# Performance work log

Measured on AMD Instinct MI355X. Metric: run time of the kernel, lower is better.

The kernel has to match this reference:

```python
import jax, jax.numpy as jnp
import numpy as np
from jax import lax

LB, UB = 0.0, 0.1
N_ITERS = 32  # fixed-point iterations for water-filling rebalance


def _conv(x, w, b):
    y = lax.conv_general_dilated(x, w, (1, 1), ((1, 1), (1, 1)),
                                 dimension_numbers=("NCHW", "OIHW", "NCHW"))
    return y + b[None, :, None, None]


def _maxpool2(x):
    return lax.reduce_window(x, -jnp.inf, lax.max, (1, 1, 2, 2), (1, 1, 2, 2), "VALID")


def _linear(x, w, b):
    return x @ w.T + b


def _gru(x_num, W_ih, W_hh, b_ih, b_hh):
    # x_num: [B, S, N]; torch GRU gate order r, z, n
    B = x_num.shape[0]
    H = W_hh.shape[1]
    xs = jnp.swapaxes(x_num, 0, 1)  # [S, B, N]

    def step(h, x_t):
        gi = x_t @ W_ih.T + b_ih            # [B, 3H]
        gh = h @ W_hh.T + b_hh              # [B, 3H]
        i_r, i_z, i_n = jnp.split(gi, 3, axis=-1)
        h_r, h_z, h_n = jnp.split(gh, 3, axis=-1)
        r = jax.nn.sigmoid(i_r + h_r)
        z = jax.nn.sigmoid(i_z + h_z)
        n = jnp.tanh(i_n + r * h_n)
        h_new = (1.0 - z) * n + z * h
        return h_new, None

    h0 = jnp.zeros((B, H), dtype=x_num.dtype)
    h_last, _ = lax.scan(step, h0, xs)
    return h_last


def _rebalance_one(w):
    # vectorized fixed-point version of the per-sample while-loop water-filling
    def body(carry, _):
        old, wc = carry
        leftover = jnp.sum(old - wc)
        mask = wc != UB
        s = jnp.sum(jnp.where(mask, wc, 0.0))
        gift = jnp.where(mask & (s > 0), leftover * wc / jnp.where(s > 0, s, 1.0), 0.0)
        new_old = wc + gift
        new_wc = jnp.clip(new_old, LB, UB)
        return (new_old, new_wc), None

    init = (w, jnp.clip(w, LB, UB))
    (_, wc), _ = lax.scan(body, init, None, length=N_ITERS)
    return wc


def setup_inputs() -> dict:
    key = jax.random.key(0)
    ks = jax.random.split(key, 16)
    B, S, N, H_IMG, W_IMG, HID = 16, 60, 50, 64, 60, 128
    fc_in = 64 * (H_IMG // 4) * (W_IMG // 4)  # 15360
    sc = 0.05
    return {
        "x_num": jax.random.normal(ks[0], (B, S, N), jnp.float32),
        "x_img": jax.random.uniform(ks[1], (B, N, H_IMG, W_IMG), jnp.float32),
        "conv1_w": jax.random.normal(ks[2], (32, 1, 3, 3), jnp.float32) * sc,
        "conv1_b": jnp.zeros((32,), jnp.float32),
        "conv2_w": jax.random.normal(ks[3], (64, 32, 3, 3), jnp.float32) * sc,
        "conv2_b": jnp.zeros((64,), jnp.float32),
        "fc1_w": jax.random.normal(ks[4], (64, fc_in), jnp.float32) * 0.01,
        "fc1_b": jnp.zeros((64,), jnp.float32),
        "fc_binary_w": jax.random.normal(ks[5], (1, 64), jnp.float32) * sc,
        "fc_binary_b": jnp.zeros((1,), jnp.float32),
        "fc2_w": jax.random.normal(ks[6], (128, 64), jnp.float32) * sc,
        "fc2_b": jnp.zeros((128,), jnp.float32),
        "W_ih": jax.random.normal(ks[7], (3 * HID, N), jnp.float32) * sc,
        "W_hh": jax.random.normal(ks[8], (3 * HID, HID), jnp.float32) * sc,
        "b_ih": jnp.zeros((3 * HID,), jnp.float32),
        "b_hh": jnp.zeros((3 * HID,), jnp.float32),
        "gru_fc_w": jax.random.normal(ks[9], (N, HID), jnp.float32) * sc,
        "gru_fc_b": jnp.zeros((N,), jnp.float32),
        "fusion_w": jax.random.normal(ks[10], (64, N + 128), jnp.float32) * sc,
        "fusion_b": jnp.zeros((64,), jnp.float32),
        "final_w": jax.random.normal(ks[11], (N, 64), jnp.float32) * sc,
        "final_b": jnp.zeros((N,), jnp.float32),
    }


def reference(x_num, x_img, conv1_w, conv1_b, conv2_w, conv2_b, fc1_w, fc1_b,
              fc_binary_w, fc_binary_b, fc2_w, fc2_b, W_ih, W_hh, b_ih, b_hh,
              gru_fc_w, gru_fc_b, fusion_w, fusion_b, final_w, final_b):
    B, S, N = x_num.shape
    # GRU branch: last hidden -> Linear -> [B, N]
    h_last = _gru(x_num, W_ih, W_hh, b_ih, b_hh)
    numerical_features = _linear(h_last, gru_fc_w, gru_fc_b)

    # CNN branch on per-stock chart images
    xi = x_img.reshape(B * N, 1, x_img.shape[2], x_img.shape[3])
    h = _maxpool2(jax.nn.relu(_conv(xi, conv1_w, conv1_b)))
    h = _maxpool2(jax.nn.relu(_conv(h, conv2_w, conv2_b)))
    h = h.reshape(B * N, -1)
    feats = jax.nn.relu(_linear(h, fc1_w, fc1_b))
    binary_pred = jax.nn.sigmoid(_linear(feats, fc_binary_w, fc_binary_b))
    cnn_features = _linear(feats, fc2_w, fc2_b).reshape(B, N, -1).mean(axis=1)

    fused = jax.nn.relu(_linear(jnp.concatenate([numerical_features, cnn_features], axis=1), fusion_w, fusion_b))
    w = jax.nn.softmax(_linear(fused, final_w, final_b), axis=1)
    portfolio_weights = jax.vmap(_rebalance_one)(w)
    return portfolio_weights, binary_pred.reshape(B, N)
```

## Files before the change

### kernel.cpp

```cpp
#include <hip/hip_runtime.h>
#include <hip/hip_bf16.h>

typedef unsigned short ushort_t;
typedef short short8_t __attribute__((ext_vector_type(8)));
typedef float f32x4 __attribute__((ext_vector_type(4)));
typedef float f32x16 __attribute__((ext_vector_type(16)));
typedef ushort_t us4_t __attribute__((ext_vector_type(4)));

#define NBATCH 16
#define SEQ    60
#define NSTK   50
#define HID    128
#define G3     384
#define NIMG   800
#define IH     64
#define IW     60
#define P1H    32
#define P1W    30
#define P2C    64
#define FCIN   15360

#define OFF_WHHF   0u
#define OFF_WPREP  24576u
#define OFF_WFC1   33792u
#define OFF_GI     525312u
#define OFF_HLAST  893952u
#define OFF_POOL2  896000u
#define OFF_FC2O   7040000u
#define OFF_PART   7142400u
#define WS_FLOATS  7961600u

#define E_WHH  49152
#define E_WPR  18432
#define E_FC1  983040
#define E_TOT  (E_WHH + E_WPR + E_FC1)

struct __align__(16) ConvS {
    ushort_t pool1t[32][4][32][8];
    union {
        float    imgp[64][60];
        ushort_t pool2s[64][120];
    } u;
};
struct __align__(16) GruS {
    float    gh[16 * 388];
    ushort_t hb[16 * 136];
};
#define SMEM_BYTES 80896

__device__ __forceinline__ float fast_sig(float x) {
    const float e = __expf(-x);
    return __builtin_amdgcn_rcpf(1.f + e);
}
__device__ __forceinline__ float fast_tanh(float x) {
    const float xc = fmaxf(fminf(x, 15.f), -15.f);
    const float e = __expf(2.f * xc);
    return (e - 1.f) * __builtin_amdgcn_rcpf(e + 1.f);
}

__global__ __launch_bounds__(384) void k_pre(const float* __restrict__ xnum,
                                             const float* __restrict__ wih,
                                             const float* __restrict__ bih,
                                             const float* __restrict__ whh,
                                             const float* __restrict__ c2w,
                                             const float* __restrict__ fc1w,
                                             float* __restrict__ GI,
                                             ushort_t* __restrict__ whhf,
                                             ushort_t* __restrict__ wprep,
                                             ushort_t* __restrict__ wfc1)
{
    const int bid = blockIdx.x;
    if (bid < 960) {
        const int s = bid >> 4, b = bid & 15;
        const int j = threadIdx.x;
        const float* xr = xnum + (size_t)(b * SEQ + s) * NSTK;
        const float* wr = wih + (size_t)j * NSTK;
        float a = bih[j];
        #pragma unroll 10
        for (int k = 0; k < NSTK; ++k) a = fmaf(xr[k], wr[k], a);
        GI[((size_t)s * 16 + b) * G3 + j] = a;
        return;
    }
    const int idx = (bid - 960) * 384 + threadIdx.x;
    if (idx < E_WHH) {
        const int e = idx;
        const int i = e & 7, l = (e >> 3) & 63, ksj = e >> 9;
        const int ks = ksj & 3, jt = ksj >> 2;
        const int j = jt * 16 + (l & 15);
        const int k = ks * 32 + ((l >> 4) << 3) + i;
        __hip_bfloat16 hv = __float2bfloat16(whh[j * HID + k]);
        whhf[e] = *(ushort_t*)&hv;
    } else if (idx < E_WHH + E_WPR) {
        const int e = idx - E_WHH;
        const int i = e & 7, l = (e >> 3) & 63, rest = e >> 9;
        const int ks = rest & 1, mt = rest >> 1;
        const int tap = mt % 9, mm = mt / 9;
        const int oc = mm * 32 + (l & 31);
        const int ic = ks * 16 + ((l >> 5) << 3) + i;
        __hip_bfloat16 hv = __float2bfloat16(c2w[((size_t)oc * 32 + ic) * 9 + tap]);
        wprep[e] = *(ushort_t*)&hv;
    } else if (idx < E_TOT) {
        const int e = idx - (E_WHH + E_WPR);
        const int i = e & 7, l = (e >> 3) & 63, rest = e >> 9;
        const int n = rest & 3, T = rest >> 2;
        const int oc = n * 16 + (l & 15);
        const int k = T * 32 + ((l >> 4) << 3) + i;
        __hip_bfloat16 hv = __float2bfloat16(fc1w[(size_t)oc * FCIN + k]);
        wfc1[e] = *(ushort_t*)&hv;
    }
}

__global__ __launch_bounds__(512, 2) void k_mega(const float* __restrict__ x_img,
                                                 const float* __restrict__ c1w,
                                                 const float* __restrict__ c1b,
                                                 const float* __restrict__ c2b,
                                                 const ushort_t* __restrict__ wprep,
                                                 const float* __restrict__ GI,
                                                 const ushort_t* __restrict__ whhf,
                                                 const float* __restrict__ bhh,
                                                 ushort_t* __restrict__ pool2,
                                                 float* __restrict__ hlast)
{
    extern __shared__ char smraw[];
    const int tid = threadIdx.x;
    const int bid = blockIdx.x;

    if (bid == 0) {
        GruS* g = (GruS*)smraw;
        const int w = tid >> 6, l = tid & 63;
        const int arow = l & 15, kq = l >> 4;
        short8_t wfr[3][4];
        #pragma unroll
        for (int jj = 0; jj < 3; ++jj)
            #pragma unroll
            for (int ks = 0; ks < 4; ++ks)
                wfr[jj][ks] = *(const short8_t*)&whhf[((((w * 3 + jj) * 4 + ks) * 64 + l) * 8)];

        const int b = tid >> 5, hh0 = (tid & 31) * 4;
        const f32x4 bhr = *(const f32x4*)&bhh[hh0];
        const f32x4 bhz = *(const f32x4*)&bhh[128 + hh0];
        const f32x4 bhn = *(const f32x4*)&bhh[256 + hh0];
        float h0 = 0.f, h1 = 0.f, h2 = 0.f, h3 = 0.f;
        for (int i = tid; i < 1088; i += 512) ((unsigned int*)g->hb)[i] = 0u;
        const float* gi0 = GI + b * G3 + hh0;
        f32x4 cr = *(const f32x4*)(gi0);
        f32x4 cz = *(const f32x4*)(gi0 + 128);
        f32x4 cn = *(const f32x4*)(gi0 + 256);
        __syncthreads();

        for (int s = 0; s < SEQ; ++s) {
            const int sn = (s + 1 < SEQ) ? s + 1 : s;
            const float* gnx = GI + ((size_t)sn * 16 + b) * G3 + hh0;
            const f32x4 nr = *(const f32x4*)(gnx);
            const f32x4 nz = *(const f32x4*)(gnx + 128);
            const f32x4 nn = *(const f32x4*)(gnx + 256);

            #pragma unroll
            for (int jj = 0; jj < 3; ++jj) {
                f32x4 a = {0.f, 0.f, 0.f, 0.f};
                #pragma unroll
                for (int ks = 0; ks < 4; ++ks) {
                    short8_t af = *(const short8_t*)&g->hb[arow * 136 + ks * 32 + kq * 8];
                    a = __builtin_amdgcn_mfma_f32_16x16x32_bf16(af, wfr[jj][ks], a, 0, 0, 0);
                }
                const int jt = w * 3 + jj;
                #pragma unroll
                for (int r = 0; r < 4; ++r)
                    g->gh[(kq * 4 + r) * 388 + jt * 16 + arow] = a[r];
            }
            __syncthreads();

            const f32x4 gr = *(const f32x4*)&g->gh[b * 388 + hh0];
            const f32x4 gz = *(const f32x4*)&g->gh[b * 388 + 128 + hh0];
            const f32x4 gn = *(const f32x4*)&g->gh[b * 388 + 256 + hh0];
            float hv0, hv1, hv2, hv3;
            {
                const float r0 = fast_sig(cr[0] + gr[0] + bhr[0]);
                const float z0 = fast_sig(cz[0] + gz[0] + bhz[0]);
                const float n0 = fast_tanh(cn[0] + r0 * (gn[0] + bhn[0]));
                hv0 = (1.f - z0) * n0 + z0 * h0;
                const float r1 = fast_sig(cr[1] + gr[1] + bhr[1]);
                const float z1 = fast_sig(cz[1] + gz[1] + bhz[1]);
                const float n1 = fast_tanh(cn[1] + r1 * (gn[1] + bhn[1]));
                hv1 = (1.f - z1) * n1 + z1 * h1;
                const float r2 = fast_sig(cr[2] + gr[2] + bhr[2]);
                const float z2 = fast_sig(cz[2] + gz[2] + bhz[2]);
                const float n2 = fast_tanh(cn[2] + r2 * (gn[2] + bhn[2]));
                hv2 = (1.f - z2) * n2 + z2 * h2;
                const float r3 = fast_sig(cr[3] + gr[3] + bhr[3]);
                const float z3 = fast_sig(cz[3] + gz[3] + bhz[3]);
                const float n3 = fast_tanh(cn[3] + r3 * (gn[3] + bhn[3]));
                hv3 = (1.f - z3) * n3 + z3 * h3;
            }
            h0 = hv0; h1 = hv1; h2 = hv2; h3 = hv3;
            us4_t hp;
            { __hip_bfloat16 t0 = __float2bfloat16(h0); hp[0] = *(ushort_t*)&t0; }
            { __hip_bfloat16 t1 = __float2bfloat16(h1); hp[1] = *(ushort_t*)&t1; }
            { __hip_bfloat16 t2 = __float2bfloat16(h2); hp[2] = *(ushort_t*)&t2; }
            { __hip_bfloat16 t3 = __float2bfloat16(h3); hp[3] = *(ushort_t*)&t3; }
            *(us4_t*)&g->hb[b * 136 + hh0] = hp;
            cr = nr; cz = nz; cn = nn;
            __syncthreads();
        }
        f32x4 ho = {h0, h1, h2, h3};
        *(f32x4*)&hlast[b * HID + hh0] = ho;
        return;
    }

    ConvS* c = (ConvS*)smraw;
    const int img = bid - 1;
    const float* xim = x_img + (size_t)img * (IH * IW);

    if (tid < 256) {
        const int y = tid >> 3, cg = (tid >> 1) & 3, xs = (tid & 1) * 31;
        short8_t z = {0, 0, 0, 0, 0, 0, 0, 0};
        *(short8_t*)&c->pool1t[y][cg][xs][0] = z;
    }
    {
        const f32x4* src = (const f32x4*)xim;
        f32x4* dst = (f32x4*)c->u.imgp;
        for (int i = tid; i < 960; i += 512) dst[i] = src[i];
    }
    __syncthreads();

    #pragma unroll
    for (int rep = 0; rep < 2; ++rep) {
        const int p = tid + rep * 512;
        if (p < 960) {
            const int py = p / 30, px = p - py * 30;
            float patch[4][4];
            #pragma unroll
            for (int yy = 0; yy < 4; ++yy) {
                const int iy = 2 * py - 1 + yy;
                #pragma unroll
                for (int xx = 0; xx < 4; ++xx) {
                    const int ix = 2 * px - 1 + xx;
                    patch[yy][xx] = (iy >= 0 && iy < IH && ix >= 0 && ix < IW)
                                        ? c->u.imgp[iy][ix] : 0.f;
                }
            }
            #pragma unroll
            for (int cg = 0; cg < 4; ++cg) {
                short8_t outv;
                #pragma unroll
                for (int ch8 = 0; ch8 < 8; ++ch8) {
                    const int ch = cg * 8 + ch8;
                    float wr[9];
                    #pragma unroll
                    for (int q = 0; q < 9; ++q) wr[q] = c1w[ch * 9 + q];
                    const float bia = c1b[ch];
                    float best = 0.f;
                    #pragma unroll
                    for (int dy = 0; dy < 2; ++dy)
                        #pragma unroll
                        for (int dx = 0; dx < 2; ++dx) {
                            float sv = 0.f;
                            #pragma unroll
                            for (int ky = 0; ky < 3; ++ky)
                                #pragma unroll
                                for (int kx = 0; kx < 3; ++kx)
                                    sv = fmaf(patch[dy + ky][dx + kx], wr[ky * 3 + kx], sv);
                            best = fmaxf(best, sv + bia);
                        }
                    __hip_bfloat16 hv = __float2bfloat16(best);
                    outv[ch8] = *(short*)&hv;
                }
                *(short8_t*)&c->pool1t[py][cg][px + 1][0] = outv;
            }
        }
    }
    __syncthreads();

    {
        const int w  = tid >> 6, l = tid & 63;
        const int m  = w & 1;
        const int hi = l >> 5;
        const int col = l & 31;

        short8_t af[9][2];
        #pragma unroll
        for (int tap = 0; tap < 9; ++tap)
            #pragma unroll
            for (int ks = 0; ks < 2; ++ks)
                af[tap][ks] = *(const short8_t*)&wprep[(((m * 9 + tap) * 2 + ks) * 64 + l) * 8];
        float bia[16];
        #pragma unroll
        for (int r = 0; r < 16; ++r)
            bia[r] = c2b[m * 32 + (r & 3) + 8 * (r >> 2) + 4 * hi];

        const bool wr = ((col & 1) == 0) && (col < 30);
        const int px = col >> 1;
        const short8_t bfz = {0, 0, 0, 0, 0, 0, 0, 0};

        #pragma unroll
        for (int ph = 0; ph < 2; ++ph) {
            #pragma unroll
            for (int yy = 0; yy < 2; ++yy) {
                const int yp = ph * 8 + (w >> 1) + yy * 4;
                f32x16 a0, a1;
                #pragma unroll
                for (int r = 0; r < 16; ++r) { a0[r] = 0.f; a1[r] = 0.f; }
                #pragma unroll
                for (int ro = 0; ro < 4; ++ro) {
                    const int y = 2 * yp - 1 + ro;
                    short8_t bf[3][2];
                    if (y >= 0 && y < 32) {
                        #pragma unroll
                        for (int kx = 0; kx < 3; ++kx)
                            #pragma unroll
                            for (int ks = 0; ks < 2; ++ks)
                                bf[kx][ks] = *(const short8_t*)&c->pool1t[y][ks * 2 + hi][kx + col][0];
                    } else {
                        #pragma unroll
                        for (int kx = 0; kx < 3; ++kx)
                            #pragma unroll
                            for (int ks = 0; ks < 2; ++ks) bf[kx][ks] = bfz;
                    }
                    if (ro < 3) {
                        #pragma unroll
                        for (int kx = 0; kx < 3; ++kx)
                            #pragma unroll
                            for (int ks = 0; ks < 2; ++ks)
                                a0 = __builtin_amdgcn_mfma_f32_32x32x16_bf16(af[ro * 3 + kx][ks], bf[kx][ks], a0, 0, 0, 0);
                    }
                    if (ro >= 1) {
                        #pragma unroll
                        for (int kx = 0; kx < 3; ++kx)
                            #pragma unroll
                            for (int ks = 0; ks < 2; ++ks)
                                a1 = __builtin_amdgcn_mfma_f32_32x32x16_bf16(af[(ro - 1) * 3 + kx][ks], bf[kx][ks], a1, 0, 0, 0);
                    }
                }
                #pragma unroll
                for (int r = 0; r < 16; ++r) {
                    float v = fmaxf(a0[r], a1[r]);
                    v = fmaxf(v, __shfl_xor(v, 1, 64));
                    v = fmaxf(v + bia[r], 0.f);
                    if (wr) {
                        const int oc = m * 32 + (r & 3) + 8 * (r >> 2) + 4 * hi;
                        __hip_bfloat16 hv = __float2bfloat16(v);
                        c->u.pool2s[oc][(yp & 7) * 15 + px] = *(ushort_t*)&hv;
                    }
                }
            }
            __syncthreads();
            {
                int4* dst = (int4*)(pool2 + (size_t)img * FCIN);
                const int4* src = (const int4*)c->u.pool2s;
                #pragma unroll
                for (int jj = 0; jj < 2; ++jj) {
                    const int i = tid + jj * 512;
                    if (i < 960) {
                        const int oc = i / 15, cc = i - oc * 15;
                        dst[oc * 30 + ph * 15 + cc] = src[i];
                    }
                }
            }
            __syncthreads();
        }
    }
}

__global__ __launch_bounds__(256) void k_fc1(const ushort_t* __restrict__ pool2,
                                             const ushort_t* __restrict__ wfc1,
                                             float* __restrict__ part)
{
    const int mt = blockIdx.x >> 4;
    const int ks = blockIdx.x & 15;
    const int n = threadIdx.x >> 6, l = threadIdx.x & 63;
    const int arow = l & 15, kq = l >> 4;
    const int img16 = mt * 16;
    const ushort_t* Ab = pool2 + (size_t)(img16 + arow) * FCIN + ks * 960 + kq * 8;
    const ushort_t* Bb = wfc1 + ((size_t)(ks * 30 * 4 + n) * 64 + l) * 8;
    f32x4 acc0 = {0.f, 0.f, 0.f, 0.f}, acc1 = {0.f, 0.f, 0.f, 0.f};
    #pragma unroll 5
    for (int t = 0; t < 30; t += 2) {
        const short8_t aA = *(const short8_t*)(Ab + (size_t)t * 32);
        const short8_t bA = *(const short8_t*)(Bb + (size_t)t * 2048);
        const short8_t aB = *(const short8_t*)(Ab + (size_t)(t + 1) * 32);
        const short8_t bB = *(const short8_t*)(Bb + (size_t)(t + 1) * 2048);
        acc0 = __builtin_amdgcn_mfma_f32_16x16x32_bf16(aA, bA, acc0, 0, 0, 0);
        acc1 = __builtin_amdgcn_mfma_f32_16x16x32_bf16(aB, bB, acc1, 0, 0, 0);
    }
    float* dst = &part[((size_t)ks * NIMG + img16 + kq * 4) * 64 + n * 16 + arow];
    #pragma unroll
    for (int r = 0; r < 4; ++r)
        dst[(size_t)r * 64] = acc0[r] + acc1[r];
}

__device__ __forceinline__ float wave_sum(float v) {
    #pragma unroll
    for (int o = 32; o > 0; o >>= 1) v += __shfl_xor(v, o, 64);
    return v;
}
__device__ __forceinline__ float wave_max(float v) {
    #pragma unroll
    for (int o = 32; o > 0; o >>= 1) v = fmaxf(v, __shfl_xor(v, o, 64));
    return v;
}

__global__ __launch_bounds__(512) void k_post(const float* __restrict__ part,
                                              const float* __restrict__ fc1b,
                                              const float* __restrict__ fbw,
                                              const float* __restrict__ fbb,
                                              const float* __restrict__ fc2w,
                                              const float* __restrict__ fc2b,
                                              float* __restrict__ out,
                                              float* __restrict__ fc2o)
{
    const int t = threadIdx.x;
    const int im8 = t >> 6;
    const int tl = t & 63;
    const int img = blockIdx.x * 8 + im8;
    float s = fc1b[tl];
    #pragma unroll
    for (int ks = 0; ks < 16; ++ks) s += part[((size_t)ks * NIMG + img) * 64 + tl];
    const float f = fmaxf(s, 0.f);
    __shared__ float flc[8][64];
    flc[im8][tl] = f;
    const float bs = wave_sum(f * fbw[tl]);
    if (tl == 0) out[800 + img] = 1.f / (1.f + expf(-(bs + fbb[0])));
    __syncthreads();
    #pragma unroll
    for (int q = 0; q < 2; ++q) {
        const int j = tl + q * 64;
        float a2 = fc2b[j];
        #pragma unroll 8
        for (int k = 0; k < 64; ++k) a2 = fmaf(flc[im8][k], fc2w[j * 64 + k], a2);
        fc2o[(size_t)img * 128 + j] = a2;
    }
}

__global__ __launch_bounds__(64) void k_final(const float* __restrict__ hlast,
                                              const float* __restrict__ fc2o,
                                              const float* __restrict__ gw,
                                              const float* __restrict__ gb,
                                              const float* __restrict__ fw,
                                              const float* __restrict__ fb,
                                              const float* __restrict__ finw,
                                              const float* __restrict__ finb,
                                              float* __restrict__ out)
{
    const int b = blockIdx.x, t = threadIdx.x;
    __shared__ float cf[128], nf[64], fu[64];
    #pragma unroll
    for (int jj = 0; jj < 2; ++jj) {
        const int j = t + jj * 64;
        float s = 0.f;
        for (int n = 0; n < NSTK; ++n) s += fc2o[(size_t)(b * NSTK + n) * 128 + j];
        cf[j] = s * (1.0f / 50.0f);
    }
    float s = 0.f;
    if (t < NSTK) {
        s = gb[t];
        for (int k = 0; k < HID; ++k) s = fmaf(hlast[b * HID + k], gw[t * HID + k], s);
    }
    nf[t] = (t < NSTK) ? s : 0.f;
    __syncthreads();
    float f = fb[t];
    for (int k = 0; k < NSTK; ++k) f = fmaf(nf[k], fw[t * 178 + k], f);
    for (int k = 0; k < 128; ++k) f = fmaf(cf[k], fw[t * 178 + 50 + k], f);
    fu[t] = fmaxf(f, 0.f);
    __syncthreads();
    float L = -3.4e38f;
    if (t < NSTK) {
        L = finb[t];
        for (int k = 0; k < 64; ++k) L = fmaf(fu[k], finw[t * 64 + k], L);
    }
    const float m = wave_max(L);
    const float e = (t < NSTK) ? expf(L - m) : 0.f;
    const float se = wave_sum(e);
    const float wv = e / se;
    float old = wv;
    float wc = fminf(fmaxf(wv, 0.f), 0.1f);
    for (int it = 0; it < 32; ++it) {
        const float leftover = wave_sum(old - wc);
        const bool mask = (wc != 0.1f);
        const float ssum = wave_sum(mask ? wc : 0.f);
        const float gift = (mask && ssum > 0.f) ? leftover * wc / ssum : 0.f;
        old = wc + gift;
        wc = fminf(fmaxf(old, 0.f), 0.1f);
    }
    if (t < NSTK) out[b * NSTK + t] = wc;
}

extern "C" void kernel_launch(void* const* d_in, const int* in_sizes, int n_in,
                              void* d_out, int out_size, void* d_ws, size_t ws_size,
                              hipStream_t stream)
{
    const float* x_num = (const float*)d_in[0];
    const float* x_img = (const float*)d_in[1];
    const float* c1w  = (const float*)d_in[2];
    const float* c1b  = (const float*)d_in[3];
    const float* c2w  = (const float*)d_in[4];
    const float* c2b  = (const float*)d_in[5];
    const float* fc1w = (const float*)d_in[6];
    const float* fc1b = (const float*)d_in[7];
    const float* fbw  = (const float*)d_in[8];
    const float* fbb  = (const float*)d_in[9];
    const float* fc2w = (const float*)d_in[10];
    const float* fc2b = (const float*)d_in[11];
    const float* wih  = (const float*)d_in[12];
    const float* whh  = (const float*)d_in[13];
    const float* bih  = (const float*)d_in[14];
    const float* bhh  = (const float*)d_in[15];
    const float* gw   = (const float*)d_in[16];
    const float* gb   = (const float*)d_in[17];
    const float* fw   = (const float*)d_in[18];
    const float* fb   = (const float*)d_in[19];
    const float* finw = (const float*)d_in[20];
    const float* finb = (const float*)d_in[21];
    float* out = (float*)d_out;
    float* ws  = (float*)d_ws;
    if (ws_size < (size_t)WS_FLOATS * 4) return;

    ushort_t* whhf  = (ushort_t*)(ws + OFF_WHHF);
    ushort_t* wprep = (ushort_t*)(ws + OFF_WPREP);
    ushort_t* wfc1  = (ushort_t*)(ws + OFF_WFC1);
    float* GI       = ws + OFF_GI;
    float* hlast    = ws + OFF_HLAST;
    ushort_t* pool2 = (ushort_t*)(ws + OFF_POOL2);
    float* fc2o     = ws + OFF_FC2O;
    float* part     = ws + OFF_PART;

    (void)hipFuncSetAttribute(reinterpret_cast<const void*>(k_mega),
                              hipFuncAttributeMaxDynamicSharedMemorySize, SMEM_BYTES);

    k_pre   <<<960 + 2736, 384, 0, stream>>>(x_num, wih, bih, whh, c2w, fc1w,
                                             GI, whhf, wprep, wfc1);
    k_mega  <<<NIMG + 1, 512, SMEM_BYTES, stream>>>(x_img, c1w, c1b, c2b, wprep,
                                                    GI, whhf, bhh, pool2, hlast);
    k_fc1   <<<50 * 16, 256, 0, stream>>>(pool2, wfc1, part);
    k_post  <<<100, 512, 0, stream>>>(part, fc1b, fbw, fbb, fc2w, fc2b, out, fc2o);
    k_final <<<NBATCH, 64, 0, stream>>>(hlast, fc2o, gw, gb, fw, fb, finw, finb, out);
}
```

Before: 153.8 us.

## Split each image's conv pipeline across two blocks with halo rows

Each image is now handled by two blocks, each computing half of the pool2 rows. Each block loads only the input rows it needs plus halo rows and recomputes the overlapping pool1 halo row. Shared memory per block drops, so launch bounds ask for three blocks per CU instead of two. The aim is more parallelism and occupancy in the conv stage. The cost is redundant halo-row conv1 work, and the single GRU block now runs alongside twice as many conv blocks.

```diff
diff --git a/kernel.cpp b/kernel.cpp
--- a/kernel.cpp
+++ b/kernel.cpp
@@ -36,9 +36,9 @@
 #define E_TOT  (E_WHH + E_WPR + E_FC1)
 
 struct __align__(16) ConvS {
-    ushort_t pool1t[32][4][32][8];
+    ushort_t pool1t[18][4][32][8];
     union {
-        float    imgp[64][60];
+        float    imgp[35][60];
         ushort_t pool2s[64][120];
     } u;
 };
@@ -46,7 +46,7 @@
     float    gh[16 * 388];
     ushort_t hb[16 * 136];
 };
-#define SMEM_BYTES 80896
+#define SMEM_BYTES 52224
 
 __device__ __forceinline__ float fast_sig(float x) {
     const float e = __expf(-x);
@@ -110,7 +110,7 @@
     }
 }
 
-__global__ __launch_bounds__(512, 2) void k_mega(const float* __restrict__ x_img,
+__global__ __launch_bounds__(512, 3) void k_mega(const float* __restrict__ x_img,
                                                  const float* __restrict__ c1w,
                                                  const float* __restrict__ c1b,
                                                  const float* __restrict__ c2b,
@@ -208,65 +208,73 @@
     }
 
     ConvS* c = (ConvS*)smraw;
-    const int img = bid - 1;
+    const int img  = (bid - 1) >> 1;
+    const int half = (bid - 1) & 1;
     const float* xim = x_img + (size_t)img * (IH * IW);
-
-    if (tid < 256) {
-        const int y = tid >> 3, cg = (tid >> 1) & 3, xs = (tid & 1) * 31;
-        short8_t z = {0, 0, 0, 0, 0, 0, 0, 0};
-        *(short8_t*)&c->pool1t[y][cg][xs][0] = z;
-    }
+    const int rowbase = 29 * half;
+
     {
-        const f32x4* src = (const f32x4*)xim;
+        const short8_t z = {0, 0, 0, 0, 0, 0, 0, 0};
+        const int zrow = half ? 17 : 0;
+        if (tid < 128) {
+            const int cg = tid >> 5, xs = tid & 31;
+            *(short8_t*)&c->pool1t[zrow][cg][xs][0] = z;
+        } else if (tid < 272) {
+            const int q = tid - 128;
+            const int ly = q / 8, cg = (q >> 1) & 3, xs = (q & 1) * 31;
+            *(short8_t*)&c->pool1t[ly][cg][xs][0] = z;
+        }
+    }
+    {
+        const f32x4* src = (const f32x4*)(xim + rowbase * IW);
         f32x4* dst = (f32x4*)c->u.imgp;
-        for (int i = tid; i < 960; i += 512) dst[i] = src[i];
+        for (int i = tid; i < 525; i += 512) dst[i] = src[i];
     }
     __syncthreads();
 
-    #pragma unroll
-    for (int rep = 0; rep < 2; ++rep) {
-        const int p = tid + rep * 512;
-        if (p < 960) {
-            const int py = p / 30, px = p - py * 30;
-            float patch[4][4];
-            #pragma unroll
-            for (int yy = 0; yy < 4; ++yy) {
-                const int iy = 2 * py - 1 + yy;
+    if (tid < 510) {
+        const int gj = tid / 30, px = tid - gj * 30;
+        const int g = half * 15 + gj;
+        const int ly = gj + 1 - half;
+        float patch[4][4];
+        #pragma unroll
+        for (int yy = 0; yy < 4; ++yy) {
+            const int giy = 2 * g - 1 + yy;
+            const int liy = giy - rowbase;
+            #pragma unroll
+            for (int xx = 0; xx < 4; ++xx) {
+                const int ix = 2 * px - 1 + xx;
+                patch[yy][xx] = (giy >= 0 && giy < IH && ix >= 0 && ix < IW)
+                                    ? c->u.imgp[liy][ix] : 0.f;
+            }
+        }
+        #pragma unroll
+        for (int cg = 0; cg < 4; ++cg) {
+            short8_t outv;
+            #pragma unroll
+            for (int ch8 = 0; ch8 < 8; ++ch8) {
+                const int ch = cg * 8 + ch8;
+                float wr[9];
                 #pragma unroll
-                for (int xx = 0; xx < 4; ++xx) {
-                    const int ix = 2 * px - 1 + xx;
-                    patch[yy][xx] = (iy >= 0 && iy < IH && ix >= 0 && ix < IW)
-                                        ? c->u.imgp[iy][ix] : 0.f;
-                }
-            }
-            #pragma unroll
-            for (int cg = 0; cg < 4; ++cg) {
-                short8_t outv;
+                for (int q = 0; q < 9; ++q) wr[q] = c1w[ch * 9 + q];
+                const float bia = c1b[ch];
+                float best = 0.f;
                 #pragma unroll
-                for (int ch8 = 0; ch8 < 8; ++ch8) {
-                    const int ch = cg * 8 + ch8;
-                    float wr[9];
+                for (int dy = 0; dy < 2; ++dy)
                     #pragma unroll
-                    for (int q = 0; q < 9; ++q) wr[q] = c1w[ch * 9 + q];
-                    const float bia = c1b[ch];
-                    float best = 0.f;
-                    #pragma unroll
-                    for (int dy = 0; dy < 2; ++dy)
+                    for (int dx = 0; dx < 2; ++dx) {
+                        float sv = 0.f;
                         #pragma unroll
-                        for (int dx = 0; dx < 2; ++dx) {
-                            float sv = 0.f;
+                        for (int ky = 0; ky < 3; ++ky)
                             #pragma unroll
-                            for (int ky = 0; ky < 3; ++ky)
-                                #pragma unroll
-                                for (int kx = 0; kx < 3; ++kx)
-                                    sv = fmaf(patch[dy + ky][dx + kx], wr[ky * 3 + kx], sv);
-                            best = fmaxf(best, sv + bia);
-                        }
-                    __hip_bfloat16 hv = __float2bfloat16(best);
-                    outv[ch8] = *(short*)&hv;
-                }
-                *(short8_t*)&c->pool1t[py][cg][px + 1][0] = outv;
-            }
+                            for (int kx = 0; kx < 3; ++kx)
+                                sv = fmaf(patch[dy + ky][dx + kx], wr[ky * 3 + kx], sv);
+                        best = fmaxf(best, sv + bia);
+                    }
+                __hip_bfloat16 hv = __float2bfloat16(best);
+                outv[ch8] = *(short*)&hv;
+            }
+            *(short8_t*)&c->pool1t[ly][cg][px + 1][0] = outv;
         }
     }
     __syncthreads();
@@ -290,73 +298,61 @@
 
         const bool wr = ((col & 1) == 0) && (col < 30);
         const int px = col >> 1;
-        const short8_t bfz = {0, 0, 0, 0, 0, 0, 0, 0};
 
         #pragma unroll
-        for (int ph = 0; ph < 2; ++ph) {
-            #pragma unroll
-            for (int yy = 0; yy < 2; ++yy) {
-                const int yp = ph * 8 + (w >> 1) + yy * 4;
-                f32x16 a0, a1;
+        for (int yy = 0; yy < 2; ++yy) {
+            const int ypl = (w >> 1) + yy * 4;
+            f32x16 a0, a1;
+            #pragma unroll
+            for (int r = 0; r < 16; ++r) { a0[r] = 0.f; a1[r] = 0.f; }
+            #pragma unroll
+            for (int ro = 0; ro < 4; ++ro) {
+                const int ly = 2 * ypl + ro;
+                short8_t bf[3][2];
                 #pragma unroll
-                for (int r = 0; r < 16; ++r) { a0[r] = 0.f; a1[r] = 0.f; }
-                #pragma unroll
-                for (int ro = 0; ro < 4; ++ro) {
-                    const int y = 2 * yp - 1 + ro;
-                    short8_t bf[3][2];
-                    if (y >= 0 && y < 32) {
+                for (int kx = 0; kx < 3; ++kx)
+                    #pragma unroll
+                    for (int ks = 0; ks < 2; ++ks)
+                        bf[kx][ks] = *(const short8_t*)&c->pool1t[ly][ks * 2 + hi][kx + col][0];
+                if (ro < 3) {
+                    #pragma unroll
+                    for (int kx = 0; kx < 3; ++kx)
                         #pragma unroll
-                        for (int kx = 0; kx < 3; ++kx)
-                            #pragma unroll
-                            for (int ks = 0; ks < 2; ++ks)
-                                bf[kx][ks] = *(const short8_t*)&c->pool1t[y][ks * 2 + hi][kx + col][0];
-                    } else {
+                        for (int ks = 0; ks < 2; ++ks)
+                            a0 = __builtin_amdgcn_mfma_f32_32x32x16_bf16(af[ro * 3 + kx][ks], bf[kx][ks], a0, 0, 0, 0);
+                }
+                if (ro >= 1) {
+                    #pragma unroll
+                    for (int kx = 0; kx < 3; ++kx)
                         #pragma unroll
-                        for (int kx = 0; kx < 3; ++kx)
-                            #pragma unroll
-                            for (int ks = 0; ks < 2; ++ks) bf[kx][ks] = bfz;
-                    }
-                    if (ro < 3) {
-                        #pragma unroll
-                        for (int kx = 0; kx < 3; ++kx)
-                            #pragma unroll
-                            for (int ks = 0; ks < 2; ++ks)
-                                a0 = __builtin_amdgcn_mfma_f32_32x32x16_bf16(af[ro * 3 + kx][ks], bf[kx][ks], a0, 0, 0, 0);
-                    }
-                    if (ro >= 1) {
-                        #pragma unroll
-                        for (int kx = 0; kx < 3; ++kx)
-                            #pragma unroll
-                            for (int ks = 0; ks < 2; ++ks)
-                                a1 = __builtin_amdgcn_mfma_f32_32x32x16_bf16(af[(ro - 1) * 3 + kx][ks], bf[kx][ks], a1, 0, 0, 0);
-                    }
+                        for (int ks = 0; ks < 2; ++ks)
+                            a1 = __builtin_amdgcn_mfma_f32_32x32x16_bf16(af[(ro - 1) * 3 + kx][ks], bf[kx][ks], a1, 0, 0, 0);
                 }
-                #pragma unroll
-                for (int r = 0; r < 16; ++r) {
-                    float v = fmaxf(a0[r], a1[r]);
-                    v = fmaxf(v, __shfl_xor(v, 1, 64));
-                    v = fmaxf(v + bia[r], 0.f);
-                    if (wr) {
-                        const int oc = m * 32 + (r & 3) + 8 * (r >> 2) + 4 * hi;
-                        __hip_bfloat16 hv = __float2bfloat16(v);
-                        c->u.pool2s[oc][(yp & 7) * 15 + px] = *(ushort_t*)&hv;
-                    }
+            }
+            #pragma unroll
+            for (int r = 0; r < 16; ++r) {
+                float v = fmaxf(a0[r], a1[r]);
+                v = fmaxf(v, __shfl_xor(v, 1, 64));
+                v = fmaxf(v + bia[r], 0.f);
+                if (wr) {
+                    const int oc = m * 32 + (r & 3) + 8 * (r >> 2) + 4 * hi;
+                    __hip_bfloat16 hv = __float2bfloat16(v);
+                    c->u.pool2s[oc][ypl * 15 + px] = *(ushort_t*)&hv;
                 }
             }
-            __syncthreads();
-            {
-                int4* dst = (int4*)(pool2 + (size_t)img * FCIN);
-                const int4* src = (const int4*)c->u.pool2s;
-                #pragma unroll
-                for (int jj = 0; jj < 2; ++jj) {
-                    const int i = tid + jj * 512;
-                    if (i < 960) {
-                        const int oc = i / 15, cc = i - oc * 15;
-                        dst[oc * 30 + ph * 15 + cc] = src[i];
-                    }
+        }
+        __syncthreads();
+        {
+            int4* dst = (int4*)(pool2 + (size_t)img * FCIN);
+            const int4* src = (const int4*)c->u.pool2s;
+            #pragma unroll
+            for (int jj = 0; jj < 2; ++jj) {
+                const int i = tid + jj * 512;
+                if (i < 960) {
+                    const int oc = i / 15, cc = i - oc * 15;
+                    dst[oc * 30 + half * 15 + cc] = src[i];
                 }
             }
-            __syncthreads();
         }
     }
 }
@@ -528,8 +524,8 @@
 
     k_pre   <<<960 + 2736, 384, 0, stream>>>(x_num, wih, bih, whh, c2w, fc1w,
                                              GI, whhf, wprep, wfc1);
-    k_mega  <<<NIMG + 1, 512, SMEM_BYTES, stream>>>(x_img, c1w, c1b, c2b, wprep,
-                                                    GI, whhf, bhh, pool2, hlast);
+    k_mega  <<<2 * NIMG + 1, 512, SMEM_BYTES, stream>>>(x_img, c1w, c1b, c2b, wprep,
+                                                        GI, whhf, bhh, pool2, hlast);
     k_fc1   <<<50 * 16, 256, 0, stream>>>(pool2, wfc1, part);
     k_post  <<<100, 512, 0, stream>>>(part, fc1b, fbw, fbb, fc2w, fc2b, out, fc2o);
     k_final <<<NBATCH, 64, 0, stream>>>(hlast, fc2o, gw, gb, fw, fb, finw, finb, out);
```

Result: faster. 148.7 us (-3.3%).
